# Kernel optimization log

Hardware: AMD Instinct MI355X
Metric: run time of the kernel (lower is better)

Reference implementation:

```python
import jax, jax.numpy as jnp
import numpy as np

INP, OUP, MIP, HEADS = 512, 512, 16, 1
SCALE = (MIP // HEADS) ** -0.5


def setup_inputs() -> dict:
    key = jax.random.key(0)
    ks = jax.random.split(key, 12)
    s = 0.05
    return {
        "x": jax.random.normal(ks[0], (32, INP, 64, 64), dtype=jnp.float32),
        "w_cv1": jax.random.normal(ks[1], (MIP, INP), dtype=jnp.float32) * s,
        "b_cv1": jax.random.normal(ks[2], (MIP,), dtype=jnp.float32) * s,
        "w_q": jax.random.normal(ks[3], (MIP, MIP), dtype=jnp.float32) * s,
        "b_q": jax.random.normal(ks[4], (MIP,), dtype=jnp.float32) * s,
        "w_k": jax.random.normal(ks[5], (MIP, MIP), dtype=jnp.float32) * s,
        "b_k": jax.random.normal(ks[6], (MIP,), dtype=jnp.float32) * s,
        "w_v": jax.random.normal(ks[7], (MIP, MIP), dtype=jnp.float32) * s,
        "b_v": jax.random.normal(ks[8], (MIP,), dtype=jnp.float32) * s,
        "w_proj": jax.random.normal(ks[9], (OUP, MIP), dtype=jnp.float32) * s,
        "b_proj": jax.random.normal(ks[10], (OUP,), dtype=jnp.float32) * s,
    }


def reference(x, w_cv1, b_cv1, w_q, b_q, w_k, b_k, w_v, b_v, w_proj, b_proj):
    n, c, h, w = x.shape
    d = MIP // HEADS
    # coordinate pooling: mean over w -> [n,c,h]; mean over h -> [n,c,w]
    x_h = x.mean(axis=3)
    x_w = x.mean(axis=2)
    # cat along length, shared 1x1 conv (cv1)
    y = jnp.concatenate([x_h, x_w], axis=2)              # [n,c,h+w]
    y = jnp.einsum('ncl,mc->nml', y, w_cv1) + b_cv1[None, :, None]
    yh, yw = y[:, :, :h], y[:, :, h:]                    # [n,mip,h], [n,mip,w]
    q = jnp.einsum('nch,mc->nmh', yh, w_q) + b_q[None, :, None]
    k = jnp.einsum('ncw,mc->nmw', yw, w_k) + b_k[None, :, None]
    v = jnp.einsum('ncw,mc->nmw', yw, w_v) + b_v[None, :, None]
    qr = q.reshape(n, HEADS, d, h)
    kr = k.reshape(n, HEADS, d, w)
    vr = v.reshape(n, HEADS, d, w)
    attn = jnp.einsum('nadh,nadw->nahw', qr, kr) * SCALE  # [n,heads,h,w]
    attn = jax.nn.softmax(attn, axis=-1)
    z = jnp.einsum('nahw,nadw->nadh', attn, vr).reshape(n, MIP, h)
    y_att = jax.nn.sigmoid(
        jnp.einsum('nmh,om->noh', z, w_proj) + b_proj[None, :, None]
    )                                                     # [n,oup,h]
    return x * y_att[:, :, :, None]
```

## Files before the change

kernel.cpp:

```cpp
#include <hip/hip_runtime.h>

#define BN 32
#define BC 512
#define BH 64
#define BW 64

typedef float vf4 __attribute__((ext_vector_type(4)));

__global__ __launch_bounds__(256) void k_means(const float* __restrict__ x,
                                               float* __restrict__ ycat) {
    int bc = blockIdx.x;
    const float4* x4 = (const float4*)(x + (size_t)bc * (BH * BW));
    __shared__ float rowsum[64];
    __shared__ float colsum[64];
    __shared__ float colpart[256][5];
    int t = threadIdx.x;

    float cx = 0.f, cy = 0.f, cz = 0.f, cw = 0.f;
    for (int i = 0; i < 4; ++i) {
        int f = t + i * 256;
        float4 v = x4[f];
        float s = v.x + v.y + v.z + v.w;
        s += __shfl_down(s, 8, 16);
        s += __shfl_down(s, 4, 16);
        s += __shfl_down(s, 2, 16);
        s += __shfl_down(s, 1, 16);
        if ((t & 15) == 0) rowsum[f >> 4] = s;
        cx += v.x; cy += v.y; cz += v.z; cw += v.w;
    }
    colpart[t][0] = cx; colpart[t][1] = cy; colpart[t][2] = cz; colpart[t][3] = cw;
    __syncthreads();
    if (t < 64) {
        int base = t >> 2, comp = t & 3;
        float s = 0.f;
        for (int g = 0; g < 16; ++g) s += colpart[base + 16 * g][comp];
        colsum[t] = s;
    }
    __syncthreads();
    if (t < 128) {
        float m = (t < 64 ? rowsum[t] : colsum[t - 64]) * (1.0f / 64.0f);
        ycat[(size_t)bc * 128 + t] = m;
    }
}

__global__ __launch_bounds__(256) void k_conv1(const float* __restrict__ ycat,
                                               const float* __restrict__ w_cv1,
                                               const float* __restrict__ b_cv1,
                                               float* __restrict__ yl) {
    int bid = blockIdx.x;
    int nl = bid >> 3, lc = bid & 7;
    int t = threadIdx.x;
    __shared__ float yc_s[512][16];
    __shared__ float w_s[16][512];

    const float4* ysrc = (const float4*)(ycat + (size_t)nl * (BC * 128));
    float4* ycdst = (float4*)&yc_s[0][0];
    for (int i = 0; i < 8; ++i) {
        int i4 = t + i * 256;
        int c = i4 >> 2, j = i4 & 3;
        ycdst[c * 4 + j] = ysrc[c * 32 + lc * 4 + j];
    }
    const float4* wsrc = (const float4*)w_cv1;
    float4* wdst = (float4*)&w_s[0][0];
    for (int i = 0; i < 8; ++i) wdst[t + i * 256] = wsrc[t + i * 256];
    __syncthreads();

    int m = t >> 4, l = t & 15;
    float acc = b_cv1[m];
    #pragma unroll 8
    for (int c = 0; c < 512; ++c) acc += w_s[m][c] * yc_s[c][l];
    yl[(size_t)nl * 2048 + m * 128 + lc * 16 + l] = acc;
}

__global__ __launch_bounds__(256) void k_score(
    const float* __restrict__ yl,
    const float* __restrict__ w_q, const float* __restrict__ b_q,
    const float* __restrict__ w_k, const float* __restrict__ b_k,
    const float* __restrict__ w_v, const float* __restrict__ b_v,
    float* __restrict__ zbuf) {
    int bid = blockIdx.x;
    int nl = bid >> 3, hc = bid & 7;
    int t = threadIdx.x;
    __shared__ float yl_s[16][128];
    __shared__ float wq_s[256], wk_s[256], wv_s[256];
    __shared__ float q_s[16][8];
    __shared__ float k_s[16][64], v_s[16][64];
    __shared__ float attn_s[8][64];

    {
        const float4* s4 = (const float4*)(yl + (size_t)nl * 2048);
        float4* d4 = (float4*)&yl_s[0][0];
        for (int i = 0; i < 2; ++i) d4[t + i * 256] = s4[t + i * 256];
        wq_s[t] = w_q[t]; wk_s[t] = w_k[t]; wv_s[t] = w_v[t];
    }
    __syncthreads();

    if (t < 128) {
        int d = t >> 3, hh = t & 7, h = hc * 8 + hh;
        float a = b_q[d];
        #pragma unroll
        for (int m = 0; m < 16; ++m) a += wq_s[d * 16 + m] * yl_s[m][h];
        q_s[d][hh] = a;
    }
    for (int i = 0; i < 4; ++i) {
        int idx = t + i * 256;
        int d = idx >> 6, ww = idx & 63;
        float ak = b_k[d], av = b_v[d];
        #pragma unroll
        for (int m = 0; m < 16; ++m) {
            float yv = yl_s[m][64 + ww];
            ak += wk_s[d * 16 + m] * yv;
            av += wv_s[d * 16 + m] * yv;
        }
        k_s[d][ww] = ak; v_s[d][ww] = av;
    }
    __syncthreads();

    for (int i = 0; i < 2; ++i) {
        int idx = t + i * 256;
        int hh = idx >> 6, ww = idx & 63;
        float s = 0.f;
        #pragma unroll
        for (int d = 0; d < 16; ++d) s += q_s[d][hh] * k_s[d][ww];
        attn_s[hh][ww] = s * 0.25f;
    }
    __syncthreads();

    {
        int r = t >> 5, lane = t & 31;
        float a0 = attn_s[r][lane], a1 = attn_s[r][lane + 32];
        float mx = fmaxf(a0, a1);
        for (int off = 16; off >= 1; off >>= 1) mx = fmaxf(mx, __shfl_xor(mx, off, 32));
        float e0 = __expf(a0 - mx), e1 = __expf(a1 - mx);
        float sm = e0 + e1;
        for (int off = 16; off >= 1; off >>= 1) sm += __shfl_xor(sm, off, 32);
        float inv = 1.0f / sm;
        attn_s[r][lane] = e0 * inv;
        attn_s[r][lane + 32] = e1 * inv;
    }
    __syncthreads();

    if (t < 128) {
        int d = t >> 3, hh = t & 7;
        float a = 0.f;
        #pragma unroll 8
        for (int ww = 0; ww < 64; ++ww) a += attn_s[hh][ww] * v_s[d][ww];
        zbuf[(size_t)nl * 1024 + d * 64 + hc * 8 + hh] = a;
    }
}

__global__ __launch_bounds__(256) void k_gatemul(
    const float* __restrict__ x, const float* __restrict__ zbuf,
    const float* __restrict__ w_proj, const float* __restrict__ b_proj,
    float* __restrict__ out) {
    int rid = blockIdx.x;
    int n = rid >> 6, cb = rid & 63;
    int t = threadIdx.x;
    __shared__ float z_s[16][64];
    __shared__ float gate_s[512];

    for (int i = 0; i < 4; ++i) {
        int idx = t + i * 256;
        ((float*)z_s)[idx] = zbuf[(size_t)n * 1024 + idx];
    }
    __syncthreads();
    #pragma unroll
    for (int i = 0; i < 2; ++i) {
        int idx = t + i * 256;
        int c = cb * 8 + (idx >> 6), hh = idx & 63;
        float a = b_proj[c];
        #pragma unroll
        for (int m = 0; m < 16; ++m) a += w_proj[c * 16 + m] * z_s[m][hh];
        gate_s[idx] = 1.0f / (1.0f + __expf(-a));
    }
    __syncthreads();

    size_t base = (size_t)rid * 8192;
    const vf4* x4 = (const vf4*)x + base;
    vf4* o4 = (vf4*)out + base;
    #pragma unroll
    for (int i = 0; i < 32; ++i) {
        int f = t + i * 256;
        float g = gate_s[f >> 4];
        vf4 v = x4[f];
        v *= g;
        __builtin_nontemporal_store(v, &o4[f]);
    }
}

extern "C" void kernel_launch(void* const* d_in, const int* in_sizes, int n_in,
                              void* d_out, int out_size, void* d_ws, size_t ws_size,
                              hipStream_t stream) {
    const float* x      = (const float*)d_in[0];
    const float* w_cv1  = (const float*)d_in[1];
    const float* b_cv1  = (const float*)d_in[2];
    const float* w_q    = (const float*)d_in[3];
    const float* b_q    = (const float*)d_in[4];
    const float* w_k    = (const float*)d_in[5];
    const float* b_k    = (const float*)d_in[6];
    const float* w_v    = (const float*)d_in[7];
    const float* b_v    = (const float*)d_in[8];
    const float* w_proj = (const float*)d_in[9];
    const float* b_proj = (const float*)d_in[10];
    float* out = (float*)d_out;

    float* ycat = (float*)d_ws;
    float* yl   = ycat + (size_t)BN * BC * 128;
    float* zbuf = yl + (size_t)BN * 2048;

    hipLaunchKernelGGL(k_means, dim3(BN * BC), dim3(256), 0, stream, x, ycat);
    hipLaunchKernelGGL(k_conv1, dim3(BN * 8), dim3(256), 0, stream,
                       ycat, w_cv1, b_cv1, yl);
    hipLaunchKernelGGL(k_score, dim3(BN * 8), dim3(256), 0, stream,
                       yl, w_q, b_q, w_k, b_k, w_v, b_v, zbuf);
    hipLaunchKernelGGL(k_gatemul, dim3(BN * 64), dim3(256), 0, stream,
                       x, zbuf, w_proj, b_proj, out);
}
```

Before: 144.6 us.

## Fuse conv1 and score kernels with per-batch spin barrier, widen means blocks

Merges the cv1 projection and attention-score kernels into one launch. The 8 blocks for each batch sync through a global atomic counter with a spin-wait, and the counter is reset by the first block of the means kernel. The means kernel now reduces 4 channels per block with one wavefront per channel, using shuffles instead of shared-memory column partials. This removes one launch and some sync overhead, at the cost of relying on all 8 blocks of a batch being co-resident for the spin barrier.

Measured after the change: 182.0 us. +25.9%, slower.

```diff
diff --git a/kernel.cpp b/kernel.cpp
--- a/kernel.cpp
+++ b/kernel.cpp
@@ -8,99 +8,111 @@
 typedef float vf4 __attribute__((ext_vector_type(4)));
 
 __global__ __launch_bounds__(256) void k_means(const float* __restrict__ x,
-                                               float* __restrict__ ycat) {
-    int bc = blockIdx.x;
-    const float4* x4 = (const float4*)(x + (size_t)bc * (BH * BW));
-    __shared__ float rowsum[64];
-    __shared__ float colsum[64];
-    __shared__ float colpart[256][5];
+                                               float* __restrict__ ycat,
+                                               unsigned* __restrict__ flags) {
+    int b4 = blockIdx.x;
     int t = threadIdx.x;
+    if (b4 == 0 && t < BN) flags[t] = 0u;
+    int w = t >> 6, j = t & 63;
+    const vf4* x4 = (const vf4*)(x + ((size_t)b4 * 4 + w) * (BH * BW));
+    __shared__ float red[4][128];
 
     float cx = 0.f, cy = 0.f, cz = 0.f, cw = 0.f;
-    for (int i = 0; i < 4; ++i) {
-        int f = t + i * 256;
-        float4 v = x4[f];
+    #pragma unroll
+    for (int i = 0; i < 16; ++i) {
+        vf4 v = x4[j + 64 * i];
         float s = v.x + v.y + v.z + v.w;
         s += __shfl_down(s, 8, 16);
         s += __shfl_down(s, 4, 16);
         s += __shfl_down(s, 2, 16);
         s += __shfl_down(s, 1, 16);
-        if ((t & 15) == 0) rowsum[f >> 4] = s;
+        if ((j & 15) == 0) red[w][(j >> 4) + 4 * i] = s * (1.0f / 64.0f);
         cx += v.x; cy += v.y; cz += v.z; cw += v.w;
     }
-    colpart[t][0] = cx; colpart[t][1] = cy; colpart[t][2] = cz; colpart[t][3] = cw;
-    __syncthreads();
-    if (t < 64) {
-        int base = t >> 2, comp = t & 3;
-        float s = 0.f;
-        for (int g = 0; g < 16; ++g) s += colpart[base + 16 * g][comp];
-        colsum[t] = s;
-    }
-    __syncthreads();
-    if (t < 128) {
-        float m = (t < 64 ? rowsum[t] : colsum[t - 64]) * (1.0f / 64.0f);
-        ycat[(size_t)bc * 128 + t] = m;
-    }
-}
-
-__global__ __launch_bounds__(256) void k_conv1(const float* __restrict__ ycat,
-                                               const float* __restrict__ w_cv1,
-                                               const float* __restrict__ b_cv1,
-                                               float* __restrict__ yl) {
-    int bid = blockIdx.x;
-    int nl = bid >> 3, lc = bid & 7;
-    int t = threadIdx.x;
-    __shared__ float yc_s[512][16];
-    __shared__ float w_s[16][512];
-
-    const float4* ysrc = (const float4*)(ycat + (size_t)nl * (BC * 128));
-    float4* ycdst = (float4*)&yc_s[0][0];
-    for (int i = 0; i < 8; ++i) {
-        int i4 = t + i * 256;
-        int c = i4 >> 2, j = i4 & 3;
-        ycdst[c * 4 + j] = ysrc[c * 32 + lc * 4 + j];
-    }
-    const float4* wsrc = (const float4*)w_cv1;
-    float4* wdst = (float4*)&w_s[0][0];
-    for (int i = 0; i < 8; ++i) wdst[t + i * 256] = wsrc[t + i * 256];
-    __syncthreads();
-
-    int m = t >> 4, l = t & 15;
-    float acc = b_cv1[m];
-    #pragma unroll 8
-    for (int c = 0; c < 512; ++c) acc += w_s[m][c] * yc_s[c][l];
-    yl[(size_t)nl * 2048 + m * 128 + lc * 16 + l] = acc;
-}
-
-__global__ __launch_bounds__(256) void k_score(
-    const float* __restrict__ yl,
+    cx += __shfl_xor(cx, 16, 64); cx += __shfl_xor(cx, 32, 64);
+    cy += __shfl_xor(cy, 16, 64); cy += __shfl_xor(cy, 32, 64);
+    cz += __shfl_xor(cz, 16, 64); cz += __shfl_xor(cz, 32, 64);
+    cw += __shfl_xor(cw, 16, 64); cw += __shfl_xor(cw, 32, 64);
+    if (j < 16) {
+        vf4 cv = {cx, cy, cz, cw};
+        cv *= (1.0f / 64.0f);
+        ((vf4*)&red[w][64])[j] = cv;
+    }
+    __syncthreads();
+    size_t base = (size_t)b4 * 512;
+    #pragma unroll
+    for (int i = 0; i < 2; ++i) {
+        int idx = t + i * 256;
+        ycat[base + idx] = ((float*)red)[idx];
+    }
+}
+
+__global__ __launch_bounds__(256) void k_att(
+    const float* __restrict__ ycat,
+    const float* __restrict__ w_cv1, const float* __restrict__ b_cv1,
     const float* __restrict__ w_q, const float* __restrict__ b_q,
     const float* __restrict__ w_k, const float* __restrict__ b_k,
     const float* __restrict__ w_v, const float* __restrict__ b_v,
-    float* __restrict__ zbuf) {
+    float* __restrict__ yl, float* __restrict__ zbuf,
+    unsigned* __restrict__ flags) {
     int bid = blockIdx.x;
-    int nl = bid >> 3, hc = bid & 7;
+    int nl = bid >> 3, jc = bid & 7;
     int t = threadIdx.x;
-    __shared__ float yl_s[16][128];
-    __shared__ float wq_s[256], wk_s[256], wv_s[256];
-    __shared__ float q_s[16][8];
-    __shared__ float k_s[16][64], v_s[16][64];
-    __shared__ float attn_s[8][64];
+    __shared__ float smem[16384];
+
+    {
+        float* yc_s = smem;
+        float* w_s  = smem + 8192;
+        const float4* ysrc = (const float4*)(ycat + (size_t)nl * (BC * 128));
+        float4* ycdst = (float4*)yc_s;
+        for (int i = 0; i < 8; ++i) {
+            int i4 = t + i * 256;
+            int c = i4 >> 2, q = i4 & 3;
+            ycdst[c * 4 + q] = ysrc[c * 32 + jc * 4 + q];
+        }
+        const float4* wsrc = (const float4*)w_cv1;
+        float4* wdst = (float4*)w_s;
+        for (int i = 0; i < 8; ++i) wdst[t + i * 256] = wsrc[t + i * 256];
+        __syncthreads();
+
+        int m = t >> 4, l = t & 15;
+        float acc = b_cv1[m];
+        #pragma unroll 8
+        for (int c = 0; c < 512; ++c) acc += w_s[m * 512 + c] * yc_s[c * 16 + l];
+        yl[(size_t)nl * 2048 + m * 128 + jc * 16 + l] = acc;
+    }
+    __threadfence();
+    __syncthreads();
+    if (t == 0) {
+        atomicAdd(&flags[nl], 1u);
+        while (atomicAdd(&flags[nl], 0u) < 8u) __builtin_amdgcn_s_sleep(2);
+    }
+    __syncthreads();
+    __threadfence();
+
+    float* yl_s   = smem;
+    float* wq_s   = smem + 2048;
+    float* wk_s   = smem + 2304;
+    float* wv_s   = smem + 2560;
+    float* q_s    = smem + 2816;
+    float* k_s    = smem + 2944;
+    float* v_s    = smem + 3968;
+    float* attn_s = smem + 4992;
 
     {
         const float4* s4 = (const float4*)(yl + (size_t)nl * 2048);
-        float4* d4 = (float4*)&yl_s[0][0];
+        float4* d4 = (float4*)yl_s;
         for (int i = 0; i < 2; ++i) d4[t + i * 256] = s4[t + i * 256];
         wq_s[t] = w_q[t]; wk_s[t] = w_k[t]; wv_s[t] = w_v[t];
     }
     __syncthreads();
 
     if (t < 128) {
-        int d = t >> 3, hh = t & 7, h = hc * 8 + hh;
+        int d = t >> 3, hh = t & 7, h = jc * 8 + hh;
         float a = b_q[d];
         #pragma unroll
-        for (int m = 0; m < 16; ++m) a += wq_s[d * 16 + m] * yl_s[m][h];
-        q_s[d][hh] = a;
+        for (int m = 0; m < 16; ++m) a += wq_s[d * 16 + m] * yl_s[m * 128 + h];
+        q_s[d * 8 + hh] = a;
     }
     for (int i = 0; i < 4; ++i) {
         int idx = t + i * 256;
@@ -108,11 +120,11 @@
         float ak = b_k[d], av = b_v[d];
         #pragma unroll
         for (int m = 0; m < 16; ++m) {
-            float yv = yl_s[m][64 + ww];
+            float yv = yl_s[m * 128 + 64 + ww];
             ak += wk_s[d * 16 + m] * yv;
             av += wv_s[d * 16 + m] * yv;
         }
-        k_s[d][ww] = ak; v_s[d][ww] = av;
+        k_s[d * 64 + ww] = ak; v_s[d * 64 + ww] = av;
     }
     __syncthreads();
 
@@ -121,22 +133,22 @@
         int hh = idx >> 6, ww = idx & 63;
         float s = 0.f;
         #pragma unroll
-        for (int d = 0; d < 16; ++d) s += q_s[d][hh] * k_s[d][ww];
-        attn_s[hh][ww] = s * 0.25f;
+        for (int d = 0; d < 16; ++d) s += q_s[d * 8 + hh] * k_s[d * 64 + ww];
+        attn_s[hh * 64 + ww] = s * 0.25f;
     }
     __syncthreads();
 
     {
         int r = t >> 5, lane = t & 31;
-        float a0 = attn_s[r][lane], a1 = attn_s[r][lane + 32];
+        float a0 = attn_s[r * 64 + lane], a1 = attn_s[r * 64 + lane + 32];
         float mx = fmaxf(a0, a1);
         for (int off = 16; off >= 1; off >>= 1) mx = fmaxf(mx, __shfl_xor(mx, off, 32));
         float e0 = __expf(a0 - mx), e1 = __expf(a1 - mx);
         float sm = e0 + e1;
         for (int off = 16; off >= 1; off >>= 1) sm += __shfl_xor(sm, off, 32);
         float inv = 1.0f / sm;
-        attn_s[r][lane] = e0 * inv;
-        attn_s[r][lane + 32] = e1 * inv;
+        attn_s[r * 64 + lane] = e0 * inv;
+        attn_s[r * 64 + lane + 32] = e1 * inv;
     }
     __syncthreads();
 
@@ -144,8 +156,8 @@
         int d = t >> 3, hh = t & 7;
         float a = 0.f;
         #pragma unroll 8
-        for (int ww = 0; ww < 64; ++ww) a += attn_s[hh][ww] * v_s[d][ww];
-        zbuf[(size_t)nl * 1024 + d * 64 + hc * 8 + hh] = a;
+        for (int ww = 0; ww < 64; ++ww) a += attn_s[hh * 64 + ww] * v_s[d * 64 + ww];
+        zbuf[(size_t)nl * 1024 + d * 64 + jc * 8 + hh] = a;
     }
 }
 
@@ -207,12 +219,13 @@
     float* ycat = (float*)d_ws;
     float* yl   = ycat + (size_t)BN * BC * 128;
     float* zbuf = yl + (size_t)BN * 2048;
-
-    hipLaunchKernelGGL(k_means, dim3(BN * BC), dim3(256), 0, stream, x, ycat);
-    hipLaunchKernelGGL(k_conv1, dim3(BN * 8), dim3(256), 0, stream,
-                       ycat, w_cv1, b_cv1, yl);
-    hipLaunchKernelGGL(k_score, dim3(BN * 8), dim3(256), 0, stream,
-                       yl, w_q, b_q, w_k, b_k, w_v, b_v, zbuf);
+    unsigned* flags = (unsigned*)(zbuf + (size_t)BN * 1024);
+
+    hipLaunchKernelGGL(k_means, dim3(BN * BC / 4), dim3(256), 0, stream,
+                       x, ycat, flags);
+    hipLaunchKernelGGL(k_att, dim3(BN * 8), dim3(256), 0, stream,
+                       ycat, w_cv1, b_cv1, w_q, b_q, w_k, b_k, w_v, b_v,
+                       yl, zbuf, flags);
     hipLaunchKernelGGL(k_gatemul, dim3(BN * 64), dim3(256), 0, stream,
                        x, zbuf, w_proj, b_proj, out);
 }
```
